# Kernel optimization log

Measured on AMD Instinct MI355X. Metric: run time of the kernel, lower is better.

## Reference

```python
import jax, jax.numpy as jnp
import numpy as np

PERCENTILE_SCALING = 10.0
BIAS_SCALING = 10.0
KH = KW = 3
B, C, H, W = 16, 64, 112, 112


def setup_inputs() -> dict:
    key = jax.random.key(0)
    kx, kk = jax.random.split(key)
    x = jax.random.normal(kx, (B, C, H, W), dtype=jnp.float32)
    # trunc_normal_(mean=1.0, std=0.05) approximated by normal (values stay in range w.h.p.)
    kernel = 1.0 + 0.05 * jax.random.normal(kk, (1, C, KH, KW), dtype=jnp.float32)
    bias = jnp.zeros((C,), dtype=jnp.float32)
    percentile = jnp.zeros((C,), dtype=jnp.float32)
    return {"x": x, "kernel": kernel, "bias": bias, "percentile": percentile}


def reference(x, kernel, bias, percentile):
    b, c, h, w = x.shape
    kh, kw = kernel.shape[2], kernel.shape[3]
    ph, pw = kh // 2, kw // 2
    # pad + add scaled bias (bias is inside every window tap, matching torch order)
    xp = jnp.pad(x, ((0, 0), (0, 0), (ph, ph), (pw, pw)))
    xp = xp + (bias * BIAS_SCALING)[None, :, None, None]
    # weighted min/max over the kxk window without materializing the unfold tensor:
    # iterate the small fixed set of k*k taps, keep running max/min.
    x_max = None
    x_min = None
    for i in range(kh):
        for j in range(kw):
            tap = xp[:, :, i:i + h, j:j + w] * kernel[0, :, i, j][None, :, None, None]
            x_max = tap if x_max is None else jnp.maximum(x_max, tap)
            x_min = tap if x_min is None else jnp.minimum(x_min, tap)
    p = jax.nn.sigmoid(percentile * PERCENTILE_SCALING)[None, :, None, None]
    out = x_min + (x_max - x_min) * p
    out = out - (bias * BIAS_SCALING)[None, :, None, None]
    return out
```

## Files before the change

kernel.cpp:

```cpp
#include <hip/hip_runtime.h>
#include <math.h>


#define B_ 16
#define C_ 64
#define H_ 112
#define W_ 112
#define TW 8
#define TH 4
#define GX (W_ / TW)
#define GY (H_ / TH)

typedef float f32x4 __attribute__((ext_vector_type(4)));

__global__ __launch_bounds__(256) void morph2d_kernel(
    const float* __restrict__ x,
    const float* __restrict__ kern,
    const float* __restrict__ bias,
    const float* __restrict__ perc,
    float* __restrict__ out)
{
    const int total = B_ * C_ * GY * GX;
    int t = blockIdx.x * blockDim.x + threadIdx.x;
    if (t >= total) return;

    int gx = t % GX;
    int r1 = t / GX;
    int ys = r1 % GY;
    int bc = r1 / GY;
    int c  = bc % C_;

    float biasv = bias[c] * 10.0f;
    float p = 1.0f / (1.0f + expf(-perc[c] * 10.0f));

    const float* plane  = x   + (size_t)bc * (H_ * W_);
    float*       oplane = out + (size_t)bc * (H_ * W_);
    const int x0 = gx * TW;
    const int y0 = ys * TH;

    float s[TH + 2][TW + 2];
    #pragma unroll
    for (int i = 0; i < TH + 2; ++i) {
        int yy = y0 + i - 1;
        if ((unsigned)yy < (unsigned)H_) {
            const float* rp = plane + yy * W_ + x0;
            f32x4 a  = *reinterpret_cast<const f32x4*>(rp);
            f32x4 b4 = *reinterpret_cast<const f32x4*>(rp + 4);
            s[i][1] = a.x;  s[i][2] = a.y;  s[i][3] = a.z;  s[i][4] = a.w;
            s[i][5] = b4.x; s[i][6] = b4.y; s[i][7] = b4.z; s[i][8] = b4.w;
            s[i][0] = (x0 > 0)       ? rp[-1] : 0.0f;
            s[i][9] = (x0 + TW < W_) ? rp[TW] : 0.0f;
        } else {
            #pragma unroll
            for (int j = 0; j < TW + 2; ++j) s[i][j] = 0.0f;
        }
    }

    float k[9], bk[9];
    #pragma unroll
    for (int i = 0; i < 9; ++i) {
        k[i]  = kern[c * 9 + i];
        bk[i] = k[i] * biasv;
    }

    #pragma unroll
    for (int r = 0; r < TH; ++r) {
        float o[TW];
        #pragma unroll
        for (int q = 0; q < TW; ++q) {
            float t0 = fmaf(s[r][q],     k[0], bk[0]);
            float t1 = fmaf(s[r][q + 1], k[1], bk[1]);
            float t2 = fmaf(s[r][q + 2], k[2], bk[2]);
            float vmax = fmaxf(fmaxf(t0, t1), t2);
            float vmin = fminf(fminf(t0, t1), t2);
            t0 = fmaf(s[r + 1][q],     k[3], bk[3]);
            t1 = fmaf(s[r + 1][q + 1], k[4], bk[4]);
            t2 = fmaf(s[r + 1][q + 2], k[5], bk[5]);
            vmax = fmaxf(vmax, fmaxf(fmaxf(t0, t1), t2));
            vmin = fminf(vmin, fminf(fminf(t0, t1), t2));
            t0 = fmaf(s[r + 2][q],     k[6], bk[6]);
            t1 = fmaf(s[r + 2][q + 1], k[7], bk[7]);
            t2 = fmaf(s[r + 2][q + 2], k[8], bk[8]);
            vmax = fmaxf(vmax, fmaxf(fmaxf(t0, t1), t2));
            vmin = fminf(vmin, fminf(fminf(t0, t1), t2));
            o[q] = fmaf(vmax - vmin, p, vmin) - biasv;
        }

        float* orow = oplane + (y0 + r) * W_ + x0;
        f32x4 lo = { o[0], o[1], o[2], o[3] };
        f32x4 hi = { o[4], o[5], o[6], o[7] };
        __builtin_nontemporal_store(lo, reinterpret_cast<f32x4*>(orow));
        __builtin_nontemporal_store(hi, reinterpret_cast<f32x4*>(orow + 4));
    }
}

extern "C" void kernel_launch(void* const* d_in, const int* in_sizes, int n_in,
                              void* d_out, int out_size, void* d_ws, size_t ws_size,
                              hipStream_t stream) {
    const float* x    = (const float*)d_in[0];
    const float* kern = (const float*)d_in[1];
    const float* bias = (const float*)d_in[2];
    const float* perc = (const float*)d_in[3];
    float* out = (float*)d_out;

    const int total = B_ * C_ * GY * GX;
    const int block = 256;
    const int grid  = (total + block - 1) / block;
    morph2d_kernel<<<grid, block, 0, stream>>>(x, kern, bias, perc, out);
}
```

Before: 26.03 us.

## Map 14-lane groups to row strips and exchange halo columns via wave shuffles

Threads are regrouped so each 64-lane wave covers four row strips of 14 lanes, with 8 lanes idle. Horizontal halo values now come from neighbouring lanes through shuffles instead of extra scalar global loads. Row loads are clamped and masked rather than branched, so every lane issues the same vector loads. The idea is to cut redundant unaligned halo loads and branch divergence, at the cost of leaving 12.5% of lanes unused and adding shuffle instructions.

```diff
diff --git a/kernel.cpp b/kernel.cpp
--- a/kernel.cpp
+++ b/kernel.cpp
@@ -10,6 +10,8 @@
 #define TH 4
 #define GX (W_ / TW)
 #define GY (H_ / TH)
+#define STRIPS (B_ * C_ * GY)
+#define WAVES (STRIPS / 4)
 
 typedef float f32x4 __attribute__((ext_vector_type(4)));
 
@@ -20,18 +22,27 @@
     const float* __restrict__ perc,
     float* __restrict__ out)
 {
-    const int total = B_ * C_ * GY * GX;
-    int t = blockIdx.x * blockDim.x + threadIdx.x;
-    if (t >= total) return;
+    const int tid  = blockIdx.x * blockDim.x + threadIdx.x;
+    const int wave = tid >> 6;
+    const int lane = tid & 63;
+    const int sub  = lane / 14;
+    const int gx   = lane % 14;
+    if (sub >= 4) return;
 
-    int gx = t % GX;
-    int r1 = t / GX;
-    int ys = r1 % GY;
-    int bc = r1 / GY;
-    int c  = bc % C_;
+    const int strip = wave * 4 + sub;
+    const int ys = strip % GY;
+    const int bc = strip / GY;
+    const int c  = bc & (C_ - 1);
 
-    float biasv = bias[c] * 10.0f;
-    float p = 1.0f / (1.0f + expf(-perc[c] * 10.0f));
+    const float biasv = bias[c] * 10.0f;
+    const float p = 1.0f / (1.0f + expf(-perc[c] * 10.0f));
+
+    float k[9], bk[9];
+    #pragma unroll
+    for (int i = 0; i < 9; ++i) {
+        k[i]  = kern[c * 9 + i];
+        bk[i] = k[i] * biasv;
+    }
 
     const float* plane  = x   + (size_t)bc * (H_ * W_);
     float*       oplane = out + (size_t)bc * (H_ * W_);
@@ -41,26 +52,20 @@
     float s[TH + 2][TW + 2];
     #pragma unroll
     for (int i = 0; i < TH + 2; ++i) {
-        int yy = y0 + i - 1;
-        if ((unsigned)yy < (unsigned)H_) {
-            const float* rp = plane + yy * W_ + x0;
-            f32x4 a  = *reinterpret_cast<const f32x4*>(rp);
-            f32x4 b4 = *reinterpret_cast<const f32x4*>(rp + 4);
-            s[i][1] = a.x;  s[i][2] = a.y;  s[i][3] = a.z;  s[i][4] = a.w;
-            s[i][5] = b4.x; s[i][6] = b4.y; s[i][7] = b4.z; s[i][8] = b4.w;
-            s[i][0] = (x0 > 0)       ? rp[-1] : 0.0f;
-            s[i][9] = (x0 + TW < W_) ? rp[TW] : 0.0f;
-        } else {
-            #pragma unroll
-            for (int j = 0; j < TW + 2; ++j) s[i][j] = 0.0f;
-        }
-    }
-
-    float k[9], bk[9];
-    #pragma unroll
-    for (int i = 0; i < 9; ++i) {
-        k[i]  = kern[c * 9 + i];
-        bk[i] = k[i] * biasv;
+        int yy  = y0 + i - 1;
+        int yyc = yy < 0 ? 0 : (yy > H_ - 1 ? H_ - 1 : yy);
+        const float* rp = plane + yyc * W_ + x0;
+        f32x4 a  = *reinterpret_cast<const f32x4*>(rp);
+        f32x4 b4 = *reinterpret_cast<const f32x4*>(rp + 4);
+        const bool inY = ((unsigned)yy < (unsigned)H_);
+        s[i][1] = inY ? a.x  : 0.0f;  s[i][2] = inY ? a.y  : 0.0f;
+        s[i][3] = inY ? a.z  : 0.0f;  s[i][4] = inY ? a.w  : 0.0f;
+        s[i][5] = inY ? b4.x : 0.0f;  s[i][6] = inY ? b4.y : 0.0f;
+        s[i][7] = inY ? b4.z : 0.0f;  s[i][8] = inY ? b4.w : 0.0f;
+        float left  = __shfl_up(s[i][8], 1);
+        float right = __shfl_down(s[i][1], 1);
+        s[i][0] = (gx > 0)      ? left  : 0.0f;
+        s[i][9] = (gx < GX - 1) ? right : 0.0f;
     }
 
     #pragma unroll
@@ -103,8 +108,8 @@
     const float* perc = (const float*)d_in[3];
     float* out = (float*)d_out;
 
-    const int total = B_ * C_ * GY * GX;
+    const int threads = WAVES * 64;
     const int block = 256;
-    const int grid  = (total + block - 1) / block;
+    const int grid  = threads / block;
     morph2d_kernel<<<grid, block, 0, stream>>>(x, kern, bias, perc, out);
 }
```

Result: slower. 32.17 us (+23.6%).

## Use 4x4 per-thread tiles with lane shuffles for horizontal halo exchange

Applied to the files above, without the earlier changes.

Each thread now computes a 4x4 output tile instead of 4x8. Groups of 32 lanes cover one 4-row strip of a plane (28 active lanes), and the left/right halo columns come from neighbouring lanes via __shfl_up/__shfl_down rather than separate scalar global loads. Vertical halo rows are clamped so loads never go out of bounds, and are zeroed afterwards. The aim is fully vectorized, coalesced loads with no scalar halo reads and more threads in flight. The cost is 4 of every 32 lanes idling, plus shuffle overhead and a higher vertical-halo read ratio per output.

```diff
diff --git a/kernel.cpp b/kernel.cpp
--- a/kernel.cpp
+++ b/kernel.cpp
@@ -6,10 +6,6 @@
 #define C_ 64
 #define H_ 112
 #define W_ 112
-#define TW 8
-#define TH 4
-#define GX (W_ / TW)
-#define GY (H_ / TH)
 
 typedef float f32x4 __attribute__((ext_vector_type(4)));
 
@@ -20,41 +16,19 @@
     const float* __restrict__ perc,
     float* __restrict__ out)
 {
-    const int total = B_ * C_ * GY * GX;
-    int t = blockIdx.x * blockDim.x + threadIdx.x;
-    if (t >= total) return;
+    const int t      = blockIdx.x * blockDim.x + threadIdx.x;
+    const int lane32 = t & 31;
+    const int group  = t >> 5;
+    const bool active = (lane32 < 28);
+    const int gx = active ? lane32 : 27;
+    const int ytile = group % 28;
+    const int bc    = group / 28;
+    const int c     = bc & (C_ - 1);
+    const int x0 = gx * 4;
+    const int y0 = ytile * 4;
 
-    int gx = t % GX;
-    int r1 = t / GX;
-    int ys = r1 % GY;
-    int bc = r1 / GY;
-    int c  = bc % C_;
-
-    float biasv = bias[c] * 10.0f;
-    float p = 1.0f / (1.0f + expf(-perc[c] * 10.0f));
-
-    const float* plane  = x   + (size_t)bc * (H_ * W_);
-    float*       oplane = out + (size_t)bc * (H_ * W_);
-    const int x0 = gx * TW;
-    const int y0 = ys * TH;
-
-    float s[TH + 2][TW + 2];
-    #pragma unroll
-    for (int i = 0; i < TH + 2; ++i) {
-        int yy = y0 + i - 1;
-        if ((unsigned)yy < (unsigned)H_) {
-            const float* rp = plane + yy * W_ + x0;
-            f32x4 a  = *reinterpret_cast<const f32x4*>(rp);
-            f32x4 b4 = *reinterpret_cast<const f32x4*>(rp + 4);
-            s[i][1] = a.x;  s[i][2] = a.y;  s[i][3] = a.z;  s[i][4] = a.w;
-            s[i][5] = b4.x; s[i][6] = b4.y; s[i][7] = b4.z; s[i][8] = b4.w;
-            s[i][0] = (x0 > 0)       ? rp[-1] : 0.0f;
-            s[i][9] = (x0 + TW < W_) ? rp[TW] : 0.0f;
-        } else {
-            #pragma unroll
-            for (int j = 0; j < TW + 2; ++j) s[i][j] = 0.0f;
-        }
-    }
+    const float biasv = bias[c] * 10.0f;
+    const float p = 1.0f / (1.0f + __expf(-perc[c] * 10.0f));
 
     float k[9], bk[9];
     #pragma unroll
@@ -63,11 +37,38 @@
         bk[i] = k[i] * biasv;
     }
 
+    const float* plane = x + (size_t)bc * (H_ * W_);
+
+    f32x4 v[6];
     #pragma unroll
-    for (int r = 0; r < TH; ++r) {
-        float o[TW];
+    for (int i = 0; i < 6; ++i) {
+        int yy  = y0 + i - 1;
+        int yyc = yy < 0 ? 0 : (yy > H_ - 1 ? H_ - 1 : yy);
+        v[i] = *reinterpret_cast<const f32x4*>(plane + yyc * W_ + x0);
+    }
+
+    float s[6][6];
+    #pragma unroll
+    for (int i = 0; i < 6; ++i) {
+        int yy = y0 + i - 1;
+        const bool inY = ((unsigned)yy < (unsigned)H_);
+        float rx = inY ? v[i].x : 0.0f;
+        float ry = inY ? v[i].y : 0.0f;
+        float rz = inY ? v[i].z : 0.0f;
+        float rw = inY ? v[i].w : 0.0f;
+        float left  = __shfl_up(rw, 1);
+        float right = __shfl_down(rx, 1);
+        s[i][0] = (gx > 0)  ? left  : 0.0f;
+        s[i][1] = rx; s[i][2] = ry; s[i][3] = rz; s[i][4] = rw;
+        s[i][5] = (gx < 27) ? right : 0.0f;
+    }
+
+    float* oplane = out + (size_t)bc * (H_ * W_);
+    #pragma unroll
+    for (int r = 0; r < 4; ++r) {
+        float o[4];
         #pragma unroll
-        for (int q = 0; q < TW; ++q) {
+        for (int q = 0; q < 4; ++q) {
             float t0 = fmaf(s[r][q],     k[0], bk[0]);
             float t1 = fmaf(s[r][q + 1], k[1], bk[1]);
             float t2 = fmaf(s[r][q + 2], k[2], bk[2]);
@@ -85,12 +86,11 @@
             vmin = fminf(vmin, fminf(fminf(t0, t1), t2));
             o[q] = fmaf(vmax - vmin, p, vmin) - biasv;
         }
-
-        float* orow = oplane + (y0 + r) * W_ + x0;
-        f32x4 lo = { o[0], o[1], o[2], o[3] };
-        f32x4 hi = { o[4], o[5], o[6], o[7] };
-        __builtin_nontemporal_store(lo, reinterpret_cast<f32x4*>(orow));
-        __builtin_nontemporal_store(hi, reinterpret_cast<f32x4*>(orow + 4));
+        if (active) {
+            f32x4 ov = { o[0], o[1], o[2], o[3] };
+            __builtin_nontemporal_store(
+                ov, reinterpret_cast<f32x4*>(oplane + (y0 + r) * W_ + x0));
+        }
     }
 }
 
@@ -103,8 +103,8 @@
     const float* perc = (const float*)d_in[3];
     float* out = (float*)d_out;
 
-    const int total = B_ * C_ * GY * GX;
+    const int threads = (B_ * C_ * 28) * 32;
     const int block = 256;
-    const int grid  = (total + block - 1) / block;
+    const int grid  = threads / block;
     morph2d_kernel<<<grid, block, 0, stream>>>(x, kern, bias, perc, out);
 }
```

New measurement: 22.85 us. 12.2% less time.
